# Kernel optimization log

Hardware: AMD Instinct MI355X
Metric: run time of the kernel (lower is better)

Reference implementation:

```python
import jax, jax.numpy as jnp
import numpy as np

BETA = 0.25  # commitment_weight


def _conv(x, w, b=None, stride=1, pad=0):
    y = jax.lax.conv_general_dilated(x, w, (stride, stride), ((pad, pad), (pad, pad)),
                                     dimension_numbers=('NCHW', 'OIHW', 'NCHW'))
    return y if b is None else y + b[None, :, None, None]


def _convT(x, w, b):
    # PyTorch ConvTranspose2d(kernel=4, stride=2, padding=1); w stored as (in, out, 4, 4)
    wf = jnp.flip(w, (2, 3)).transpose(1, 0, 2, 3)  # -> OIHW, spatially flipped
    y = jax.lax.conv_general_dilated(x, wf, (1, 1), ((2, 2), (2, 2)), lhs_dilation=(2, 2),
                                     dimension_numbers=('NCHW', 'OIHW', 'NCHW'))
    return y + b[None, :, None, None]


def _res(x, wa, wb):
    # ResidualLayer: x + conv1x1(relu(conv3x3(x))) , both convs bias-free
    return x + _conv(jax.nn.relu(_conv(x, wa, pad=1)), wb)


def _lrelu(x):
    return jax.nn.leaky_relu(x, 0.01)


def setup_inputs() -> dict:
    key = jax.random.key(0)
    ks = iter(jax.random.split(key, 32))
    def p(shape, s=0.05):
        return jax.random.normal(next(ks), shape, jnp.float32) * s
    inp = {
        'inputs': jax.random.normal(next(ks), (16, 4, 256, 256), jnp.float32),
        # encoder
        'e1_w': p((64, 4, 4, 4)),    'e1_b': p((64,)),
        'e2_w': p((128, 64, 4, 4)),  'e2_b': p((128,)),
        'e3_w': p((128, 128, 3, 3)), 'e3_b': p((128,)),
        'r1a_w': p((128, 128, 3, 3)), 'r1b_w': p((128, 128, 1, 1)),
        'r2a_w': p((128, 128, 3, 3)), 'r2b_w': p((128, 128, 1, 1)),
        'e4_w': p((64, 128, 1, 1)),  'e4_b': p((64,)),
        # residual VQ codebooks: (num_quantizers, codebook_size, dim)
        'codebooks': p((4, 512, 64), 1.0),
        # decoder
        'd1_w': p((128, 64, 3, 3)),  'd1_b': p((128,)),
        'dr1a_w': p((128, 128, 3, 3)), 'dr1b_w': p((128, 128, 1, 1)),
        'dr2a_w': p((128, 128, 3, 3)), 'dr2b_w': p((128, 128, 1, 1)),
        'dt1_w': p((128, 64, 4, 4)), 'dt1_b': p((64,)),  # (in, out, kH, kW) torch layout
        'dt2_w': p((64, 4, 4, 4)),   'dt2_b': p((4,)),
    }
    return inp


def reference(inputs, e1_w, e1_b, e2_w, e2_b, e3_w, e3_b, r1a_w, r1b_w, r2a_w, r2b_w,
              e4_w, e4_b, codebooks, d1_w, d1_b, dr1a_w, dr1b_w, dr2a_w, dr2b_w,
              dt1_w, dt1_b, dt2_w, dt2_b):
    # ---- encoder ----
    h = _lrelu(_conv(inputs, e1_w, e1_b, 2, 1))
    h = _lrelu(_conv(h, e2_w, e2_b, 2, 1))
    h = _lrelu(_conv(h, e3_w, e3_b, 1, 1))
    h = _res(h, r1a_w, r1b_w)
    h = _res(h, r2a_w, r2b_w)
    h = _lrelu(h)
    h = _lrelu(_conv(h, e4_w, e4_b, 1, 0))
    # ---- residual vector quantization ----
    z = h.transpose(0, 2, 3, 1)                     # B,H,W,D
    B, H, W, D = z.shape
    r = z.reshape(-1, D)                            # N,D tokens
    q_out = jnp.zeros_like(r)
    idx_list, losses = [], []
    for i in range(codebooks.shape[0]):
        cb = codebooks[i]                           # K,D
        d = (r * r).sum(-1, keepdims=True) - 2.0 * (r @ cb.T) + (cb * cb).sum(-1)
        idx = jnp.argmin(d, axis=-1)                # N
        q = cb[idx]                                 # N,D gather
        losses.append(BETA * jnp.mean((jax.lax.stop_gradient(q) - r) ** 2))
        q_st = r + jax.lax.stop_gradient(q - r)     # straight-through
        q_out = q_out + q_st
        r = r - jax.lax.stop_gradient(q)            # residual for next stage
        idx_list.append(idx)
    indices = jnp.stack(idx_list, -1).reshape(B, H, W, -1)   # B,H,W,Q
    losses = jnp.stack(losses)                                # (Q,)
    qz = q_out.reshape(B, H, W, D).transpose(0, 3, 1, 2)      # B,D,H,W
    # ---- decoder ----
    h = _lrelu(_conv(qz, d1_w, d1_b, 1, 1))
    h = _res(h, dr1a_w, dr1b_w)
    h = _res(h, dr2a_w, dr2b_w)
    h = _lrelu(h)
    h = _lrelu(_convT(h, dt1_w, dt1_b))
    recons = jax.nn.relu(_convT(h, dt2_w, dt2_b))
    return recons, indices, losses
```

## Files before the change

kernel.cpp:

```cpp
#include <hip/hip_runtime.h>
#include <cstddef>


template<int ACT> __device__ __forceinline__ float actf(float v) {
    if constexpr (ACT == 1) return v > 0.f ? v : 0.f;
    else if constexpr (ACT == 2) return v > 0.f ? v : 0.01f * v;
    else return v;
}
__device__ __forceinline__ float lrelu_in(float v) { return v > 0.f ? v : 0.01f * v; }

template<int CIN, int COUT, int K, int S, int P, int HIN, int WIN, int HOUT, int WOUT,
         int ICC, int NPY, int ACT, bool BIAS>
__launch_bounds__(256, (NPY >= 4 ? 2 : 4))
__global__ void conv_k(const float* __restrict__ in, const float* __restrict__ w,
                       const float* __restrict__ bias, float* __restrict__ out)
{
    constexpr int K2 = K * K;
    constexpr int NR = S * (NPY - 1) + K;
    constexpr int BH = 16 * NPY;
    __shared__ float sw[ICC * K2 * 16];
    const int tid = threadIdx.x;
    const int tx = tid & 15, ty = tid >> 4;
    constexpr int TW = WOUT / 16;
    const int bx = blockIdx.x % TW, by = blockIdx.x / TW;
    const int ox = bx * 16 + tx;
    const int oy0 = by * BH + ty * NPY;
    const int oc0 = blockIdx.y * 16;
    const int n = blockIdx.z;
    const int ix0 = ox * S - P, iy0 = oy0 * S - P;

    int ro[NR]; float mr[NR];
#pragma unroll
    for (int r = 0; r < NR; ++r) {
        const int iy = iy0 + r;
        const bool v = (iy >= 0) && (iy < HIN);
        ro[r] = v ? iy * WIN : 0;
        mr[r] = v ? 1.f : 0.f;
    }
    int co[K]; float mc[K];
#pragma unroll
    for (int c = 0; c < K; ++c) {
        const int ix = ix0 + c;
        const bool v = (ix >= 0) && (ix < WIN);
        co[c] = v ? ix : 0;
        mc[c] = v ? 1.f : 0.f;
    }

    float acc[NPY][16];
#pragma unroll
    for (int py = 0; py < NPY; ++py)
#pragma unroll
        for (int j = 0; j < 16; ++j) acc[py][j] = 0.f;

    for (int ic0 = 0; ic0 < CIN; ic0 += ICC) {
        __syncthreads();
        for (int t = tid; t < ICC * K2 * 16; t += 256) {
            int oc_l = t & 15, r = t >> 4, k = r % K2, ic_l = r / K2;
            sw[(ic_l * K2 + k) * 16 + oc_l] =
                w[((size_t)(oc0 + oc_l) * CIN + ic0 + ic_l) * K2 + k];
        }
        __syncthreads();
#pragma unroll 1
        for (int ic_l = 0; ic_l < ICC; ++ic_l) {
            const float* ip = in + (size_t)(n * CIN + ic0 + ic_l) * HIN * WIN;
            float patch[NR][K];
#pragma unroll
            for (int r = 0; r < NR; ++r)
#pragma unroll
                for (int c = 0; c < K; ++c)
                    patch[r][c] = ip[ro[r] + co[c]] * (mr[r] * mc[c]);
            const float* swp = &sw[ic_l * K2 * 16];
#pragma unroll
            for (int ky = 0; ky < K; ++ky) {
#pragma unroll
                for (int kx = 0; kx < K; ++kx) {
                    const float4* wp = (const float4*)&swp[(ky * K + kx) * 16];
                    float4 w0 = wp[0], w1 = wp[1], w2 = wp[2], w3 = wp[3];
#pragma unroll
                    for (int py = 0; py < NPY; ++py) {
                        const float v = patch[py * S + ky][kx];
                        acc[py][0]  = fmaf(w0.x, v, acc[py][0]);
                        acc[py][1]  = fmaf(w0.y, v, acc[py][1]);
                        acc[py][2]  = fmaf(w0.z, v, acc[py][2]);
                        acc[py][3]  = fmaf(w0.w, v, acc[py][3]);
                        acc[py][4]  = fmaf(w1.x, v, acc[py][4]);
                        acc[py][5]  = fmaf(w1.y, v, acc[py][5]);
                        acc[py][6]  = fmaf(w1.z, v, acc[py][6]);
                        acc[py][7]  = fmaf(w1.w, v, acc[py][7]);
                        acc[py][8]  = fmaf(w2.x, v, acc[py][8]);
                        acc[py][9]  = fmaf(w2.y, v, acc[py][9]);
                        acc[py][10] = fmaf(w2.z, v, acc[py][10]);
                        acc[py][11] = fmaf(w2.w, v, acc[py][11]);
                        acc[py][12] = fmaf(w3.x, v, acc[py][12]);
                        acc[py][13] = fmaf(w3.y, v, acc[py][13]);
                        acc[py][14] = fmaf(w3.z, v, acc[py][14]);
                        acc[py][15] = fmaf(w3.w, v, acc[py][15]);
                    }
                }
            }
        }
    }
#pragma unroll
    for (int py = 0; py < NPY; ++py) {
#pragma unroll
        for (int j = 0; j < 16; ++j) {
            float r = acc[py][j];
            if (BIAS) r += bias[oc0 + j];
            r = actf<ACT>(r);
            out[((size_t)(n * COUT + oc0 + j) * HOUT + oy0 + py) * WOUT + ox] = r;
        }
    }
}

template<int CIN, int COUT, int NPX, int ACT, bool BIAS, bool INL, bool RESID, bool TOK>
__launch_bounds__(256, 3)
__global__ void conv1x1_k(const float* __restrict__ in, const float* __restrict__ w,
                          const float* __restrict__ bias, const float* __restrict__ resid,
                          float* __restrict__ out)
{
    constexpr int HW = 4096;
    __shared__ float sw[16 * CIN];
    const int tid = threadIdx.x;
    const int base = blockIdx.x * (256 * NPX) + tid;
    const int oc0 = blockIdx.y * 16;
    const int n = blockIdx.z;

    for (int t = tid; t < 16 * CIN; t += 256) {
        int oc_l = t & 15, ic = t >> 4;
        sw[ic * 16 + oc_l] = w[(size_t)(oc0 + oc_l) * CIN + ic];
    }
    __syncthreads();

    float acc[NPX][16];
#pragma unroll
    for (int p = 0; p < NPX; ++p)
#pragma unroll
        for (int j = 0; j < 16; ++j) acc[p][j] = 0.f;

    const float* ip = in + (size_t)n * CIN * HW;
#pragma unroll 2
    for (int ic = 0; ic < CIN; ++ic) {
        float v[NPX];
#pragma unroll
        for (int p = 0; p < NPX; ++p) {
            float t = ip[(size_t)ic * HW + base + 256 * p];
            if (INL) t = lrelu_in(t);
            v[p] = t;
        }
        const float4* wp = (const float4*)&sw[ic * 16];
#pragma unroll
        for (int q4 = 0; q4 < 4; ++q4) {
            const float4 wv = wp[q4];
#pragma unroll
            for (int p = 0; p < NPX; ++p) {
                acc[p][q4 * 4 + 0] = fmaf(wv.x, v[p], acc[p][q4 * 4 + 0]);
                acc[p][q4 * 4 + 1] = fmaf(wv.y, v[p], acc[p][q4 * 4 + 1]);
                acc[p][q4 * 4 + 2] = fmaf(wv.z, v[p], acc[p][q4 * 4 + 2]);
                acc[p][q4 * 4 + 3] = fmaf(wv.w, v[p], acc[p][q4 * 4 + 3]);
            }
        }
    }
#pragma unroll
    for (int p = 0; p < NPX; ++p) {
        const int pix = base + 256 * p;
#pragma unroll
        for (int j = 0; j < 16; ++j) {
            float r = acc[p][j];
            if (BIAS) r += bias[oc0 + j];
            r = actf<ACT>(r);
            if (RESID) r += resid[((size_t)(n * COUT + oc0 + j)) * HW + pix];
            if (TOK)
                out[((size_t)n * HW + pix) * COUT + oc0 + j] = r;
            else
                out[((size_t)(n * COUT + oc0 + j)) * HW + pix] = r;
        }
    }
}

template<int CIN, int COUT, int OCT, int HIN, int ICC, int ACT, bool INL>
__launch_bounds__(256, 3)
__global__ void convt_k(const float* __restrict__ in, const float* __restrict__ w,
                        const float* __restrict__ bias, float* __restrict__ out)
{
    constexpr int WIN = HIN, HOUT = 2 * HIN, WOUT = 2 * HIN;
    __shared__ float sw[ICC * 16 * OCT];
    const int tid = threadIdx.x;
    const int tx = tid & 15, ty = tid >> 4;
    constexpr int TBW = WOUT / 32;
    const int bx = blockIdx.x % TBW, by = blockIdx.x / TBW;
    const int A = by * 16 + ty;
    const int C = bx * 16 + tx;
    const int oc0 = blockIdx.y * OCT;
    const int n = blockIdx.z;

    int offs[9]; float msk[9];
#pragma unroll
    for (int dy = 0; dy < 3; ++dy) {
#pragma unroll
        for (int dx = 0; dx < 3; ++dx) {
            const int iy = A - 1 + dy, ix = C - 1 + dx;
            const bool v = (iy >= 0) && (iy < HIN) && (ix >= 0) && (ix < WIN);
            offs[dy * 3 + dx] = v ? iy * WIN + ix : 0;
            msk[dy * 3 + dx] = v ? 1.f : 0.f;
        }
    }

    float acc[4 * OCT];
#pragma unroll
    for (int j = 0; j < 4 * OCT; ++j) acc[j] = 0.f;

    for (int ic0 = 0; ic0 < CIN; ic0 += ICC) {
        __syncthreads();
        for (int t = tid; t < ICC * 16 * OCT; t += 256) {
            int oc_l = t % OCT, r = t / OCT, k = r & 15, ic_l = r >> 4;
            sw[(ic_l * 16 + k) * OCT + oc_l] =
                w[((size_t)(ic0 + ic_l) * COUT + oc0 + oc_l) * 16 + k];
        }
        __syncthreads();
#pragma unroll 1
        for (int ic_l = 0; ic_l < ICC; ++ic_l) {
            const float* ip = in + (size_t)(n * CIN + ic0 + ic_l) * HIN * WIN;
            float in9[9];
#pragma unroll
            for (int j = 0; j < 9; ++j) {
                float v = ip[offs[j]] * msk[j];
                if (INL) v = lrelu_in(v);
                in9[j] = v;
            }
#pragma unroll
            for (int ky = 0; ky < 4; ++ky) {
                const int ry = (ky + 1) & 1;
                const int dy = 2 - ((ky + 1) >> 1);
#pragma unroll
                for (int kx = 0; kx < 4; ++kx) {
                    const int rx = (kx + 1) & 1;
                    const int dx = 2 - ((kx + 1) >> 1);
                    const float v = in9[dy * 3 + dx];
                    const int po = ry * 2 + rx;
                    const float4* wp = (const float4*)&sw[(ic_l * 16 + ky * 4 + kx) * OCT];
#pragma unroll
                    for (int q4 = 0; q4 < OCT / 4; ++q4) {
                        float4 wv = wp[q4];
                        acc[po * OCT + q4 * 4 + 0] = fmaf(wv.x, v, acc[po * OCT + q4 * 4 + 0]);
                        acc[po * OCT + q4 * 4 + 1] = fmaf(wv.y, v, acc[po * OCT + q4 * 4 + 1]);
                        acc[po * OCT + q4 * 4 + 2] = fmaf(wv.z, v, acc[po * OCT + q4 * 4 + 2]);
                        acc[po * OCT + q4 * 4 + 3] = fmaf(wv.w, v, acc[po * OCT + q4 * 4 + 3]);
                    }
                }
            }
        }
    }
#pragma unroll
    for (int po = 0; po < 4; ++po) {
        const int ry = po >> 1, rx = po & 1;
        const int oy = 2 * A + ry, ox = 2 * C + rx;
#pragma unroll
        for (int j = 0; j < OCT; ++j) {
            float r = acc[po * OCT + j] + bias[oc0 + j];
            r = actf<ACT>(r);
            out[((size_t)(n * COUT + oc0 + j) * HOUT + oy) * WOUT + ox] = r;
        }
    }
}

__global__ void norm_k(const float* __restrict__ cb, float* __restrict__ nrm) {
    const int c = blockIdx.x * 256 + threadIdx.x;
    const float4* p = (const float4*)(cb + (size_t)c * 64);
    float a0 = 0.f, a1 = 0.f, a2 = 0.f, a3 = 0.f;
#pragma unroll
    for (int i = 0; i < 16; ++i) {
        float4 v = p[i];
        a0 = fmaf(v.x, v.x, a0); a1 = fmaf(v.y, v.y, a1);
        a2 = fmaf(v.z, v.z, a2); a3 = fmaf(v.w, v.w, a3);
    }
    nrm[c] = (a0 + a1) + (a2 + a3);
}

__launch_bounds__(128)
__global__ void rvq_k(const float* __restrict__ z, const float* __restrict__ cb,
                      const float* __restrict__ nrm,
                      float* __restrict__ q, float* __restrict__ idx_out,
                      float* __restrict__ loss_acc)
{
    __shared__ float scb[128 * 64];
    __shared__ float ssc[128];
    const int tid = threadIdx.x;
    const int h = tid & 1;
    const int tloc = tid >> 1;
    const int t = blockIdx.x * 64 + tloc;

    float zr[32], r[32];
    const float4* zp = (const float4*)(z + (size_t)t * 64 + h * 32);
#pragma unroll
    for (int i = 0; i < 8; ++i) {
        float4 v = zp[i];
        zr[4 * i + 0] = v.x; zr[4 * i + 1] = v.y; zr[4 * i + 2] = v.z; zr[4 * i + 3] = v.w;
        r[4 * i + 0] = v.x;  r[4 * i + 1] = v.y;  r[4 * i + 2] = v.z;  r[4 * i + 3] = v.w;
    }

    for (int s = 0; s < 4; ++s) {
        float s0 = 0.f, s1 = 0.f, s2 = 0.f, s3 = 0.f;
#pragma unroll
        for (int i = 0; i < 32; i += 4) {
            s0 = fmaf(r[i + 0], r[i + 0], s0);
            s1 = fmaf(r[i + 1], r[i + 1], s1);
            s2 = fmaf(r[i + 2], r[i + 2], s2);
            s3 = fmaf(r[i + 3], r[i + 3], s3);
        }
        float sr2 = (s0 + s1) + (s2 + s3);
        sr2 += __shfl_xor(sr2, 1, 64);

        float dmin = 3.4e38f;
        int best = 0;
        for (int pass = 0; pass < 4; ++pass) {
            __syncthreads();
            const float* src = cb + ((size_t)s * 512 + pass * 128) * 64;
            for (int i2 = tid; i2 < 128 * 64 / 4; i2 += 128)
                ((float4*)scb)[i2] = ((const float4*)src)[i2];
            ssc[tid] = nrm[(size_t)s * 512 + pass * 128 + tid];
            __syncthreads();
#pragma unroll 2
            for (int kk = 0; kk < 128; ++kk) {
                const float4* cp = (const float4*)&scb[kk * 64 + h * 32];
                float d0 = 0.f, d1 = 0.f, d2 = 0.f, d3 = 0.f;
#pragma unroll
                for (int i = 0; i < 8; ++i) {
                    float4 c = cp[i];
                    d0 = fmaf(r[4 * i + 0], c.x, d0);
                    d1 = fmaf(r[4 * i + 1], c.y, d1);
                    d2 = fmaf(r[4 * i + 2], c.z, d2);
                    d3 = fmaf(r[4 * i + 3], c.w, d3);
                }
                float dot = (d0 + d1) + (d2 + d3);
                dot += __shfl_xor(dot, 1, 64);
                const float d = fmaf(-2.f, dot, sr2) + ssc[kk];
                if (d < dmin) { dmin = d; best = pass * 128 + kk; }
            }
        }
        float lv = (h == 0) ? dmin : 0.f;
#pragma unroll
        for (int off = 32; off; off >>= 1) lv += __shfl_down(lv, off, 64);
        if ((tid & 63) == 0) atomicAdd(&loss_acc[s], lv);

        if (h == 0) idx_out[(size_t)t * 4 + s] = (float)best;

        const float4* cbest = (const float4*)(cb + ((size_t)s * 512 + best) * 64 + h * 32);
#pragma unroll
        for (int i = 0; i < 8; ++i) {
            float4 c = cbest[i];
            r[4 * i + 0] -= c.x; r[4 * i + 1] -= c.y;
            r[4 * i + 2] -= c.z; r[4 * i + 3] -= c.w;
        }
    }
    const int n = t >> 12, pix = t & 4095;
    float* qp = q + (size_t)n * 64 * 4096 + pix;
#pragma unroll
    for (int i = 0; i < 32; ++i)
        qp[(size_t)(h * 32 + i) * 4096] = zr[i] - r[i];
}

__global__ void init_k(float* loss_acc) {
    if (threadIdx.x < 4) loss_acc[threadIdx.x] = 0.f;
}
__global__ void fin_k(const float* __restrict__ loss_acc, float* __restrict__ out_loss) {
    if (threadIdx.x < 4)
        out_loss[threadIdx.x] = loss_acc[threadIdx.x] * (0.25f / 4194304.f);
}

extern "C" void kernel_launch(void* const* d_in, const int* in_sizes, int n_in,
                              void* d_out, int out_size, void* d_ws, size_t ws_size,
                              hipStream_t stream)
{
    const float* x    = (const float*)d_in[0];
    const float* e1w  = (const float*)d_in[1];  const float* e1b = (const float*)d_in[2];
    const float* e2w  = (const float*)d_in[3];  const float* e2b = (const float*)d_in[4];
    const float* e3w  = (const float*)d_in[5];  const float* e3b = (const float*)d_in[6];
    const float* r1aw = (const float*)d_in[7];  const float* r1bw = (const float*)d_in[8];
    const float* r2aw = (const float*)d_in[9];  const float* r2bw = (const float*)d_in[10];
    const float* e4w  = (const float*)d_in[11]; const float* e4b = (const float*)d_in[12];
    const float* cbs  = (const float*)d_in[13];
    const float* d1w  = (const float*)d_in[14]; const float* d1b = (const float*)d_in[15];
    const float* dr1aw= (const float*)d_in[16]; const float* dr1bw = (const float*)d_in[17];
    const float* dr2aw= (const float*)d_in[18]; const float* dr2bw = (const float*)d_in[19];
    const float* dt1w = (const float*)d_in[20]; const float* dt1b = (const float*)d_in[21];
    const float* dt2w = (const float*)d_in[22]; const float* dt2b = (const float*)d_in[23];

    float* out = (float*)d_out;
    float* ws  = (float*)d_ws;

    float* BIG = ws;
    float* P2  = BIG;
    float* P3  = BIG + 8388608;
    float* P1  = ws + 16777216;
    float* Z   = ws + 25165824;
    float* Q   = ws + 29360128;
    float* LACC= ws + 33554432;
    float* NRM = ws + 33554448;

    float* out_recons = out;
    float* out_idx    = out + 4194304;
    float* out_loss   = out + 4194304 + 262144;

    init_k<<<1, 64, 0, stream>>>(LACC);
    norm_k<<<8, 256, 0, stream>>>(cbs, NRM);

    conv_k<4, 64, 4, 2, 1, 256, 256, 128, 128, 4, 2, 2, true>
        <<<dim3(32, 4, 16), 256, 0, stream>>>(x, e1w, e1b, BIG);
    conv_k<64, 128, 4, 2, 1, 128, 128, 64, 64, 16, 2, 2, true>
        <<<dim3(8, 8, 16), 256, 0, stream>>>(BIG, e2w, e2b, P1);
    conv_k<128, 128, 3, 1, 1, 64, 64, 64, 64, 16, 4, 2, true>
        <<<dim3(4, 8, 16), 256, 0, stream>>>(P1, e3w, e3b, P2);
    conv_k<128, 128, 3, 1, 1, 64, 64, 64, 64, 16, 4, 1, false>
        <<<dim3(4, 8, 16), 256, 0, stream>>>(P2, r1aw, nullptr, P3);
    conv1x1_k<128, 128, 4, 0, false, false, true, false>
        <<<dim3(4, 8, 16), 256, 0, stream>>>(P3, r1bw, nullptr, P2, P1);
    conv_k<128, 128, 3, 1, 1, 64, 64, 64, 64, 16, 4, 1, false>
        <<<dim3(4, 8, 16), 256, 0, stream>>>(P1, r2aw, nullptr, P3);
    conv1x1_k<128, 128, 4, 0, false, false, true, false>
        <<<dim3(4, 8, 16), 256, 0, stream>>>(P3, r2bw, nullptr, P1, P2);
    conv1x1_k<128, 64, 2, 2, true, true, false, true>
        <<<dim3(8, 4, 16), 256, 0, stream>>>(P2, e4w, e4b, nullptr, Z);

    rvq_k<<<1024, 128, 0, stream>>>(Z, cbs, NRM, Q, out_idx, LACC);
    fin_k<<<1, 64, 0, stream>>>(LACC, out_loss);

    conv_k<64, 128, 3, 1, 1, 64, 64, 64, 64, 16, 4, 2, true>
        <<<dim3(4, 8, 16), 256, 0, stream>>>(Q, d1w, d1b, P1);
    conv_k<128, 128, 3, 1, 1, 64, 64, 64, 64, 16, 4, 1, false>
        <<<dim3(4, 8, 16), 256, 0, stream>>>(P1, dr1aw, nullptr, P2);
    conv1x1_k<128, 128, 4, 0, false, false, true, false>
        <<<dim3(4, 8, 16), 256, 0, stream>>>(P2, dr1bw, nullptr, P1, P3);
    conv_k<128, 128, 3, 1, 1, 64, 64, 64, 64, 16, 4, 1, false>
        <<<dim3(4, 8, 16), 256, 0, stream>>>(P3, dr2aw, nullptr, P2);
    conv1x1_k<128, 128, 4, 0, false, false, true, false>
        <<<dim3(4, 8, 16), 256, 0, stream>>>(P2, dr2bw, nullptr, P3, P1);
    convt_k<128, 64, 16, 64, 8, 2, true>
        <<<dim3(16, 4, 16), 256, 0, stream>>>(P1, dt1w, dt1b, BIG);
    convt_k<64, 4, 4, 128, 16, 1, false>
        <<<dim3(64, 1, 16), 256, 0, stream>>>(BIG, dt2w, dt2b, out_recons);
}
```

Measured before the change: 2.892 ms.

## Restructure RVQ search: one token per lane, split codebook across waves

The residual-VQ kernel now holds the full 64-dim residual for one token in each lane and splits each stage's 512 codes across the two wavefronts, 256 codes each. Codebook entries are read straight from global memory with wave-uniform addresses (scalar/broadcast loads), replacing the staged LDS tiles and their per-pass barriers. The two waves' minima are merged through a small LDS exchange. This removes the per-code pair shuffle and the LDS staging, but raises register pressure (64-float residual) and relies on cache for codebook reads.

```diff
diff --git a/kernel.cpp b/kernel.cpp
--- a/kernel.cpp
+++ b/kernel.cpp
@@ -276,87 +276,120 @@
     nrm[c] = (a0 + a1) + (a2 + a3);
 }
 
-__launch_bounds__(128)
+__launch_bounds__(128, 2)
 __global__ void rvq_k(const float* __restrict__ z, const float* __restrict__ cb,
                       const float* __restrict__ nrm,
                       float* __restrict__ q, float* __restrict__ idx_out,
                       float* __restrict__ loss_acc)
 {
-    __shared__ float scb[128 * 64];
-    __shared__ float ssc[128];
+    __shared__ float lds_min[2][64];
+    __shared__ int   lds_idx[2][64];
     const int tid = threadIdx.x;
-    const int h = tid & 1;
-    const int tloc = tid >> 1;
-    const int t = blockIdx.x * 64 + tloc;
-
-    float zr[32], r[32];
-    const float4* zp = (const float4*)(z + (size_t)t * 64 + h * 32);
-#pragma unroll
-    for (int i = 0; i < 8; ++i) {
-        float4 v = zp[i];
-        zr[4 * i + 0] = v.x; zr[4 * i + 1] = v.y; zr[4 * i + 2] = v.z; zr[4 * i + 3] = v.w;
-        r[4 * i + 0] = v.x;  r[4 * i + 1] = v.y;  r[4 * i + 2] = v.z;  r[4 * i + 3] = v.w;
+    const int lane = tid & 63;
+    const int w = __builtin_amdgcn_readfirstlane(tid >> 6);
+    const int t = blockIdx.x * 64 + lane;
+
+    float r[64];
+    {
+        const float4* zp = (const float4*)(z + (size_t)t * 64);
+#pragma unroll
+        for (int i = 0; i < 16; ++i) {
+            float4 v = zp[i];
+            r[4 * i + 0] = v.x; r[4 * i + 1] = v.y;
+            r[4 * i + 2] = v.z; r[4 * i + 3] = v.w;
+        }
     }
 
     for (int s = 0; s < 4; ++s) {
-        float s0 = 0.f, s1 = 0.f, s2 = 0.f, s3 = 0.f;
-#pragma unroll
-        for (int i = 0; i < 32; i += 4) {
-            s0 = fmaf(r[i + 0], r[i + 0], s0);
-            s1 = fmaf(r[i + 1], r[i + 1], s1);
-            s2 = fmaf(r[i + 2], r[i + 2], s2);
-            s3 = fmaf(r[i + 3], r[i + 3], s3);
-        }
-        float sr2 = (s0 + s1) + (s2 + s3);
-        sr2 += __shfl_xor(sr2, 1, 64);
-
+        float sr2;
+        {
+            float a0 = 0.f, a1 = 0.f, a2 = 0.f, a3 = 0.f;
+            float b0 = 0.f, b1 = 0.f, b2 = 0.f, b3 = 0.f;
+#pragma unroll
+            for (int i = 0; i < 32; i += 4) {
+                a0 = fmaf(r[i + 0], r[i + 0], a0);
+                a1 = fmaf(r[i + 1], r[i + 1], a1);
+                a2 = fmaf(r[i + 2], r[i + 2], a2);
+                a3 = fmaf(r[i + 3], r[i + 3], a3);
+                b0 = fmaf(r[32 + i + 0], r[32 + i + 0], b0);
+                b1 = fmaf(r[32 + i + 1], r[32 + i + 1], b1);
+                b2 = fmaf(r[32 + i + 2], r[32 + i + 2], b2);
+                b3 = fmaf(r[32 + i + 3], r[32 + i + 3], b3);
+            }
+            sr2 = ((a0 + a1) + (a2 + a3)) + ((b0 + b1) + (b2 + b3));
+        }
+
+        const float* cbase = cb + ((size_t)s * 512 + (size_t)w * 256) * 64;
+        const float* nbase = nrm + s * 512 + w * 256;
         float dmin = 3.4e38f;
         int best = 0;
-        for (int pass = 0; pass < 4; ++pass) {
-            __syncthreads();
-            const float* src = cb + ((size_t)s * 512 + pass * 128) * 64;
-            for (int i2 = tid; i2 < 128 * 64 / 4; i2 += 128)
-                ((float4*)scb)[i2] = ((const float4*)src)[i2];
-            ssc[tid] = nrm[(size_t)s * 512 + pass * 128 + tid];
-            __syncthreads();
 #pragma unroll 2
-            for (int kk = 0; kk < 128; ++kk) {
-                const float4* cp = (const float4*)&scb[kk * 64 + h * 32];
-                float d0 = 0.f, d1 = 0.f, d2 = 0.f, d3 = 0.f;
-#pragma unroll
-                for (int i = 0; i < 8; ++i) {
-                    float4 c = cp[i];
-                    d0 = fmaf(r[4 * i + 0], c.x, d0);
-                    d1 = fmaf(r[4 * i + 1], c.y, d1);
-                    d2 = fmaf(r[4 * i + 2], c.z, d2);
-                    d3 = fmaf(r[4 * i + 3], c.w, d3);
-                }
-                float dot = (d0 + d1) + (d2 + d3);
-                dot += __shfl_xor(dot, 1, 64);
-                const float d = fmaf(-2.f, dot, sr2) + ssc[kk];
-                if (d < dmin) { dmin = d; best = pass * 128 + kk; }
-            }
-        }
-        float lv = (h == 0) ? dmin : 0.f;
-#pragma unroll
-        for (int off = 32; off; off >>= 1) lv += __shfl_down(lv, off, 64);
-        if ((tid & 63) == 0) atomicAdd(&loss_acc[s], lv);
-
-        if (h == 0) idx_out[(size_t)t * 4 + s] = (float)best;
-
-        const float4* cbest = (const float4*)(cb + ((size_t)s * 512 + best) * 64 + h * 32);
-#pragma unroll
-        for (int i = 0; i < 8; ++i) {
+        for (int kk = 0; kk < 256; ++kk) {
+            const float4* cp = (const float4*)(cbase + (size_t)kk * 64);
+            float a0 = 0.f, a1 = 0.f, a2 = 0.f, a3 = 0.f;
+            float b0 = 0.f, b1 = 0.f, b2 = 0.f, b3 = 0.f;
+#pragma unroll
+            for (int i = 0; i < 8; ++i) {
+                float4 c = cp[i];
+                a0 = fmaf(r[4 * i + 0], c.x, a0);
+                a1 = fmaf(r[4 * i + 1], c.y, a1);
+                a2 = fmaf(r[4 * i + 2], c.z, a2);
+                a3 = fmaf(r[4 * i + 3], c.w, a3);
+            }
+#pragma unroll
+            for (int i = 0; i < 8; ++i) {
+                float4 c = cp[8 + i];
+                b0 = fmaf(r[32 + 4 * i + 0], c.x, b0);
+                b1 = fmaf(r[32 + 4 * i + 1], c.y, b1);
+                b2 = fmaf(r[32 + 4 * i + 2], c.z, b2);
+                b3 = fmaf(r[32 + 4 * i + 3], c.w, b3);
+            }
+            const float dot = ((a0 + a1) + (a2 + a3)) + ((b0 + b1) + (b2 + b3));
+            const float d = fmaf(-2.f, dot, sr2) + nbase[kk];
+            if (d < dmin) { dmin = d; best = kk; }
+        }
+        best += w * 256;
+
+        lds_min[w][lane] = dmin;
+        lds_idx[w][lane] = best;
+        __syncthreads();
+        const float dA = lds_min[0][lane]; const int iA = lds_idx[0][lane];
+        const float dB = lds_min[1][lane]; const int iB = lds_idx[1][lane];
+        __syncthreads();
+        const bool takeB = dB < dA;
+        dmin = takeB ? dB : dA;
+        best = takeB ? iB : iA;
+
+        if (w == 0) {
+            idx_out[(size_t)t * 4 + s] = (float)best;
+            float lv = dmin;
+#pragma unroll
+            for (int off = 32; off; off >>= 1) lv += __shfl_down(lv, off, 64);
+            if (lane == 0) atomicAdd(&loss_acc[s], lv);
+        }
+
+        const float4* cbest = (const float4*)(cb + ((size_t)s * 512 + best) * 64);
+#pragma unroll
+        for (int i = 0; i < 16; ++i) {
             float4 c = cbest[i];
             r[4 * i + 0] -= c.x; r[4 * i + 1] -= c.y;
             r[4 * i + 2] -= c.z; r[4 * i + 3] -= c.w;
         }
     }
-    const int n = t >> 12, pix = t & 4095;
-    float* qp = q + (size_t)n * 64 * 4096 + pix;
-#pragma unroll
-    for (int i = 0; i < 32; ++i)
-        qp[(size_t)(h * 32 + i) * 4096] = zr[i] - r[i];
+
+    if (w == 0) {
+        const float4* zp = (const float4*)(z + (size_t)t * 64);
+        const int n = t >> 12, pix = t & 4095;
+        float* qp = q + (size_t)n * 64 * 4096 + pix;
+#pragma unroll
+        for (int i = 0; i < 16; ++i) {
+            float4 v = zp[i];
+            qp[(size_t)(4 * i + 0) * 4096] = v.x - r[4 * i + 0];
+            qp[(size_t)(4 * i + 1) * 4096] = v.y - r[4 * i + 1];
+            qp[(size_t)(4 * i + 2) * 4096] = v.z - r[4 * i + 2];
+            qp[(size_t)(4 * i + 3) * 4096] = v.w - r[4 * i + 3];
+        }
+    }
 }
 
 __global__ void init_k(float* loss_acc) {
```

New measurement: 2.995 ms. 3.6% more time.
